# Kernel optimization log

Hardware: AMD Instinct MI355X
Metric: run time of the kernel (lower is better)

The kernel has to match this reference:

```python
import jax, jax.numpy as jnp
import numpy as np

D = 12  # grid size per axis (self.shape = [12,12,12])
BN_EPS = 1e-5


def _scatter(feats, idx, B):
    # feats: [N, C], idx: [N, 4] = (b, z, y, x). Coords are unique -> .set is exact.
    g = jnp.zeros((B, D, D, D, feats.shape[-1]), feats.dtype)
    return g.at[idx[:, 0], idx[:, 1], idx[:, 2], idx[:, 3]].set(feats)


def _subm_conv_bn_relu(feats, idx, B, W, b, gamma, beta):
    # Submanifold 3x3x3 conv == dense SAME conv on zero-filled grid, restricted
    # to the active sites (inactive neighbors contribute zero features).
    g = _scatter(feats, idx, B)  # [B, D, D, D, Cin]
    y = jax.lax.conv_general_dilated(
        g, W, window_strides=(1, 1, 1), padding='SAME',
        dimension_numbers=('NDHWC', 'DHWIO', 'NDHWC')) + b
    f = y[idx[:, 0], idx[:, 1], idx[:, 2], idx[:, 3]]  # gather active -> [N, Cout]
    # BatchNorm1d (training mode): biased batch stats over the N active points.
    mu = f.mean(axis=0)
    var = f.var(axis=0)
    f = (f - mu) * jax.lax.rsqrt(var + BN_EPS) * gamma + beta
    return jax.nn.relu(f)


def setup_inputs() -> dict:
    key = jax.random.key(0)
    B, per, Cin = 512, 864, 16
    N = B * per
    k_feat, k_coord, kp = jax.random.split(key, 3)
    # unique active voxels per batch element
    pkeys = jax.random.split(k_coord, B)
    lin = jax.vmap(lambda k: jax.random.permutation(k, D * D * D))(pkeys)[:, :per]  # [B, per]
    z, y, x = lin // (D * D), (lin // D) % D, lin % D
    bids = jnp.broadcast_to(jnp.arange(B)[:, None], (B, per))
    indices = jnp.stack([bids, z, y, x], axis=-1).reshape(N, 4).astype(jnp.int32)
    features = jax.random.normal(k_feat, (N, Cin), dtype=jnp.float32)
    ks = jax.random.split(kp, 6)
    inp = {
        'features': features, 'indices': indices, 'batch_size': B,
        'W0': jax.random.normal(ks[0], (3, 3, 3, Cin, 64), jnp.float32) * 0.05,
        'b0': jax.random.normal(ks[1], (64,), jnp.float32) * 0.05,
        'gamma0': jnp.ones((64,), jnp.float32), 'beta0': jnp.zeros((64,), jnp.float32),
        'W1': jax.random.normal(ks[2], (3, 3, 3, 64, 128), jnp.float32) * 0.05,
        'b1': jax.random.normal(ks[3], (128,), jnp.float32) * 0.05,
        'gamma1': jnp.ones((128,), jnp.float32), 'beta1': jnp.zeros((128,), jnp.float32),
        'W2': jax.random.normal(ks[4], (3, 3, 3, 128, 64), jnp.float32) * 0.05,
        'b2': jax.random.normal(ks[5], (64,), jnp.float32) * 0.05,
        'gamma2': jnp.ones((64,), jnp.float32), 'beta2': jnp.zeros((64,), jnp.float32),
    }
    return inp


def reference(features, indices, batch_size, W0, b0, gamma0, beta0,
              W1, b1, gamma1, beta1, W2, b2, gamma2, beta2):
    B = int(batch_size)
    f = _subm_conv_bn_relu(features, indices, B, W0, b0, gamma0, beta0)
    f = _subm_conv_bn_relu(f, indices, B, W1, b1, gamma1, beta1)
    f = _subm_conv_bn_relu(f, indices, B, W2, b2, gamma2, beta2)
    g = _scatter(f, indices, B)                 # [B, D, D, D, Cout]
    return jnp.transpose(g, (0, 4, 1, 2, 3))    # spconv .dense(): [B, C, D, H, W]
```

## Files before the change

kernel.cpp:

```cpp
#include <hip/hip_runtime.h>

#define DD 12
#define VOX 1728
#define BN_EPS 1e-5f
#define BATCH 512
#define PER 864
#define PERZ 865
#define NTOT (BATCH * PER)

typedef __attribute__((ext_vector_type(8))) short short8;
typedef __attribute__((ext_vector_type(4))) float f32x4;
typedef unsigned short u16;

__device__ inline u16 f2b(float f) {
    union { float f; unsigned u; } v; v.f = f;
    unsigned r = v.u + 0x7fffu + ((v.u >> 16) & 1u);
    return (u16)(r >> 16);
}
__device__ inline float b2f(u16 h) {
    union { unsigned u; float f; } v; v.u = ((unsigned)h) << 16;
    return v.f;
}
constexpr int ilog2(int v) { return v == 1 ? 0 : 1 + ilog2(v / 2); }

__device__ __forceinline__ void async_copy16(const void* g, void* l) {
    __builtin_amdgcn_global_load_lds(
        (const __attribute__((address_space(1))) void*)g,
        (__attribute__((address_space(3))) void*)l, 16, 0, 0);
}

template<int N> __device__ __forceinline__ void wait_vm() {
    if constexpr (N == 0)       asm volatile("s_waitcnt vmcnt(0)"  ::: "memory");
    else if constexpr (N == 8)  asm volatile("s_waitcnt vmcnt(8)"  ::: "memory");
    else if constexpr (N == 10) asm volatile("s_waitcnt vmcnt(10)" ::: "memory");
    else if constexpr (N == 12) asm volatile("s_waitcnt vmcnt(12)" ::: "memory");
    else if constexpr (N == 18) asm volatile("s_waitcnt vmcnt(18)" ::: "memory");
    else static_assert(N == 0, "unhandled vmcnt value");
}

__global__ void build_map_kernel(const int* __restrict__ idx, int* __restrict__ map, int N) {
    int p = blockIdx.x * blockDim.x + threadIdx.x;
    if (p >= N) return;
    const int4 v = ((const int4*)idx)[p];
    map[v.x * VOX + (v.y * DD + v.z) * DD + v.w] = p;
}

__global__ void build_nbr_kernel(const int* __restrict__ idx, const int* __restrict__ map,
                                 u16* __restrict__ nbr, int N) {
    int p = blockIdx.x * blockDim.x + threadIdx.x;
    if (p >= N) return;
    const int4 v = ((const int4*)idx)[p];
    const int base = v.x * VOX;
    const int lb = v.x * PER;
    #pragma unroll
    for (int nk = 0; nk < 27; nk++) {
        int dz = nk / 9 - 1, dy = (nk / 3) % 3 - 1, dx = nk % 3 - 1;
        int zz = v.y + dz, yy = v.z + dy, xx = v.w + dx;
        u16 out = PER;
        if (zz >= 0 && zz < DD && yy >= 0 && yy < DD && xx >= 0 && xx < DD) {
            int q = map[base + (zz * DD + yy) * DD + xx];
            if (q >= 0) out = (u16)(q - lb);
        }
        nbr[nk * N + p] = out;
    }
    #pragma unroll
    for (int nk = 27; nk < 32; nk++) nbr[nk * N + p] = PER;
}

__global__ void transpose_w_kernel(const float* __restrict__ W, u16* __restrict__ Wt,
                                   int K, int COUT, int Kpad) {
    int i = blockIdx.x * blockDim.x + threadIdx.x;
    if (i >= K * COUT) return;
    int n = i % COUT, k = i / COUT;
    Wt[(size_t)n * Kpad + k] = f2b(W[i]);
}

__global__ void cast_bf16_kernel(const float* __restrict__ in, u16* __restrict__ out, int total4) {
    int i = blockIdx.x * blockDim.x + threadIdx.x;
    if (i >= total4) return;
    int p = i >> 2, c4 = i & 3;
    int b = p / PERZ, r = p - b * PERZ;
    ushort4 o = make_ushort4(0, 0, 0, 0);
    if (r < PER) {
        float4 v = ((const float4*)in)[(size_t)(b * PER + r) * 4 + c4];
        o.x = f2b(v.x); o.y = f2b(v.y); o.z = f2b(v.z); o.w = f2b(v.w);
    }
    ((ushort4*)out)[i] = o;
}

template<int CIN, int COUT, int BM, int WM, int WN>
__global__ __launch_bounds__(256) void conv_mfma_kernel(
    const u16* __restrict__ fin,
    const u16* __restrict__ nbr,
    const u16* __restrict__ Wt,
    const float* __restrict__ bias,
    float* __restrict__ y,
    float* __restrict__ stats) {
    constexpr int Kpad   = (27 * CIN + 63) & ~63;
    constexpr int KSTEPS = Kpad / 64;
    constexpr int L2C    = ilog2(CIN);
    constexpr int BN     = WN * 64;
    constexpr int ASLOTS = BM / 32;
    constexpr int BSLOTS = BN / 32;
    constexpr int A_OFF  = BN * 128;
    constexpr int BUFB   = (BM + BN) * 128;
    static_assert(KSTEPS >= 3, "pipeline prologue needs >=3 K-steps");
    __shared__ char smem[2 * BUFB];

    const int perx = gridDim.x >> 3;
    const int bid = (blockIdx.x & 7) * perx + (blockIdx.x >> 3);
    const int p0 = bid * BM;

    const int tid = threadIdx.x;
    const int wave = tid >> 6, lane = tid & 63;
    const int wm = wave / WN, wn = wave % WN;
    const int lq = lane >> 4, lr = lane & 15;
    const int lrow = lane >> 3;
    const int kc_d = (lane & 7) ^ (lrow & 7);

    int qvoff[ASLOTS], gbase[ASLOTS];
    #pragma unroll
    for (int i = 0; i < ASLOTS; i++) {
        int m = (wave * ASLOTS + i) * 8 + lrow;
        int p = p0 + m;
        int b = p / PER;
        qvoff[i] = (((kc_d * 8) >> L2C) * NTOT + p) * 2;
        gbase[i] = b * PERZ * CIN + ((kc_d * 8) & (CIN - 1));
    }
    int bvoff[BSLOTS];
    #pragma unroll
    for (int j = 0; j < BSLOTS; j++)
        bvoff[j] = ((wave * BSLOTS + j) * 8 + lrow) * Kpad + kc_d * 8;

    int phs[2];
    phs[0] = ((0 + lq) ^ (lr & 7)) * 16;
    phs[1] = ((4 + lq) ^ (lr & 7)) * 16;
    const int aBase = A_OFF + (wm * 64 + lr) * 128;
    const int bBase = (wn * 64 + lr) * 128;

    const f32x4 fzero = {0.f, 0.f, 0.f, 0.f};
    f32x4 acc[4][4];
    #pragma unroll
    for (int i = 0; i < 4; i++)
        #pragma unroll
        for (int j = 0; j < 4; j++) acc[i][j] = fzero;

    u16 q[ASLOTS];
    auto loadQ = [&](int step) {
        int sQ = ((step * 64) >> L2C) * (NTOT * 2);
        #pragma unroll
        for (int i = 0; i < ASLOTS; i++)
            q[i] = *(const u16*)((const char*)nbr + qvoff[i] + sQ);
    };
    auto stage = [&](int step, int bo) {
        int sG = (step * 64) & (CIN - 1);
        const u16* fs = fin + sG;
        #pragma unroll
        for (int i = 0; i < ASLOTS; i++)
            async_copy16(fs + gbase[i] + ((int)q[i] << L2C),
                         smem + bo + A_OFF + (wave * ASLOTS + i) * 1024);
        const u16* wsrc = Wt + step * 64;
        #pragma unroll
        for (int j = 0; j < BSLOTS; j++)
            async_copy16(wsrc + bvoff[j], smem + bo + (wave * BSLOTS + j) * 1024);
    };

    loadQ(0);
    stage(0, 0);
    loadQ(1);

    #pragma unroll 1
    for (int kb = 0; kb < KSTEPS; kb++) {
        if (kb + 1 < KSTEPS) {
            stage(kb + 1, ((kb + 1) & 1) * BUFB);
            if (kb + 2 < KSTEPS) {
                loadQ(kb + 2);
                wait_vm<2 * ASLOTS + BSLOTS>();
            } else {
                wait_vm<ASLOTS + BSLOTS>();
            }
        } else {
            wait_vm<0>();
        }
        __builtin_amdgcn_s_barrier();

        const int so = (kb & 1) * BUFB;
        __builtin_amdgcn_s_setprio(1);
        #pragma unroll
        for (int s = 0; s < 2; s++) {
            short8 af[4], bfr[4];
            #pragma unroll
            for (int i = 0; i < 4; i++)
                af[i] = *(const short8*)(smem + so + aBase + i * 2048 + phs[s]);
            #pragma unroll
            for (int j = 0; j < 4; j++)
                bfr[j] = *(const short8*)(smem + so + bBase + j * 2048 + phs[s]);
            #pragma unroll
            for (int i = 0; i < 4; i++)
                #pragma unroll
                for (int j = 0; j < 4; j++)
                    acc[i][j] = __builtin_amdgcn_mfma_f32_16x16x32_bf16(af[i], bfr[j], acc[i][j], 0, 0, 0);
        }
        __builtin_amdgcn_s_setprio(0);
        asm volatile("s_waitcnt lgkmcnt(0)" ::: "memory");
        __builtin_amdgcn_s_barrier();
    }

    #pragma unroll
    for (int j = 0; j < 4; j++) {
        int col = wn * 64 + j * 16 + lr;
        float bv = bias[col];
        float s = 0.f, s2 = 0.f;
        #pragma unroll
        for (int i = 0; i < 4; i++) {
            int row0 = p0 + wm * 64 + i * 16 + lq * 4;
            #pragma unroll
            for (int r = 0; r < 4; r++) {
                float v = acc[i][j][r] + bv;
                y[(size_t)(row0 + r) * COUT + col] = v;
                s += v; s2 += v * v;
            }
        }
        s  += __shfl_down(s, 32);  s  += __shfl_down(s, 16);
        s2 += __shfl_down(s2, 32); s2 += __shfl_down(s2, 16);
        if (lane < 16) {
            atomicAdd(&stats[col], s);
            atomicAdd(&stats[COUT + col], s2);
        }
    }
}

template<int COUT>
__global__ void finalize_kernel(const float* __restrict__ stats, const float* __restrict__ gamma,
                                const float* __restrict__ beta, float* __restrict__ ss, int N) {
    int co = threadIdx.x;
    float inv_n = 1.f / (float)N;
    float mu  = stats[co] * inv_n;
    float var = stats[COUT + co] * inv_n - mu * mu;
    float sc  = gamma[co] * rsqrtf(var + BN_EPS);
    ss[co]        = sc;
    ss[COUT + co] = beta[co] - mu * sc;
}

template<int COUT>
__global__ void apply_kernel(const float* __restrict__ y, const float* __restrict__ ss,
                             u16* __restrict__ f, int total4) {
    int i = blockIdx.x * blockDim.x + threadIdx.x;
    if (i >= total4) return;
    constexpr int E4 = COUT / 4;
    int p = i / E4, k = i - p * E4;
    int b = p / PERZ, r = p - b * PERZ;
    ushort4 o = make_ushort4(0, 0, 0, 0);
    if (r < PER) {
        float4 v = ((const float4*)y)[(size_t)(b * PER + r) * E4 + k];
        int c0 = k * 4;
        float a;
        a = fmaf(v.x, ss[c0 + 0], ss[COUT + c0 + 0]); o.x = f2b(a > 0.f ? a : 0.f);
        a = fmaf(v.y, ss[c0 + 1], ss[COUT + c0 + 1]); o.y = f2b(a > 0.f ? a : 0.f);
        a = fmaf(v.z, ss[c0 + 2], ss[COUT + c0 + 2]); o.z = f2b(a > 0.f ? a : 0.f);
        a = fmaf(v.w, ss[c0 + 3], ss[COUT + c0 + 3]); o.w = f2b(a > 0.f ? a : 0.f);
    }
    ((ushort4*)f)[i] = o;
}

__global__ void output_kernel(const u16* __restrict__ f, const int* __restrict__ map,
                              float* __restrict__ out, int total) {
    int i = blockIdx.x * blockDim.x + threadIdx.x;
    if (i >= total) return;
    int voxel = i % VOX;
    int bc    = i / VOX;
    int c = bc & 63;
    int b = bc >> 6;
    int p = map[b * VOX + voxel];
    float v = 0.f;
    if (p >= 0) {
        int r = p - b * PER;
        v = b2f(f[(size_t)(b * PERZ + r) * 64 + c]);
    }
    out[i] = v;
}

__global__ void output_fused_kernel(const float* __restrict__ y, const float* __restrict__ ss,
                                    const int* __restrict__ map, float* __restrict__ out) {
    __shared__ float tile[64][65];
    __shared__ int   prow[64];
    const int chunk = blockIdx.x;
    const int b  = chunk / (VOX / 64);
    const int v0 = (chunk % (VOX / 64)) * 64;
    const int t = threadIdx.x;
    if (t < 64) prow[t] = map[b * VOX + v0 + t];
    __syncthreads();
    const int c = t & 63;
    const float sc = ss[c], sh = ss[64 + c];
    for (int v = t >> 6; v < 64; v += 4) {
        int p = prow[v];
        float val = 0.f;
        if (p >= 0) {
            float a = fmaf(y[(size_t)p * 64 + c], sc, sh);
            val = a > 0.f ? a : 0.f;
        }
        tile[v][c] = val;
    }
    __syncthreads();
    const int vv = t & 63;
    #pragma unroll
    for (int cc = t >> 6; cc < 64; cc += 4)
        out[(size_t)(b * 64 + cc) * VOX + v0 + vv] = tile[vv][cc];
}

extern "C" void kernel_launch(void* const* d_in, const int* in_sizes, int n_in,
                              void* d_out, int out_size, void* d_ws, size_t ws_size,
                              hipStream_t stream) {
    const float* feats = (const float*)d_in[0];
    const int*   idx   = (const int*)  d_in[1];
    const float* W0 = (const float*)d_in[3];
    const float* b0 = (const float*)d_in[4];
    const float* g0 = (const float*)d_in[5];
    const float* e0 = (const float*)d_in[6];
    const float* W1 = (const float*)d_in[7];
    const float* b1 = (const float*)d_in[8];
    const float* g1 = (const float*)d_in[9];
    const float* e1 = (const float*)d_in[10];
    const float* W2 = (const float*)d_in[11];
    const float* b2 = (const float*)d_in[12];
    const float* g2 = (const float*)d_in[13];
    const float* e2 = (const float*)d_in[14];

    const int N = in_sizes[0] / 16;

    char* ws = (char*)d_ws;
    size_t off = 0;
    auto alloc = [&](size_t bytes) { void* p = ws + off; off = (off + bytes + 255) & ~(size_t)255; return p; };
    int*   map   = (int*)  alloc((size_t)BATCH * VOX * 4);
    float* stats = (float*)alloc(3 * 256 * 4);
    float* ss    = (float*)alloc(3 * 256 * 4);
    u16*   nbr   = (u16*)  alloc((size_t)N * 32 * 2);
    u16*   wt0   = (u16*)  alloc((size_t)64  * 448  * 2);
    u16*   wt1   = (u16*)  alloc((size_t)128 * 1728 * 2);
    u16*   wt2   = (u16*)  alloc((size_t)64  * 3456 * 2);
    u16*   fbuf  = (u16*)  alloc((size_t)BATCH * PERZ * 128 * 2);
    float* y = (float*)d_out;

    const size_t y3_bytes = (size_t)N * 64 * 4;
    float* y3 = nullptr;
    if (off + y3_bytes <= ws_size) y3 = (float*)alloc(y3_bytes);

    hipMemsetAsync(map,   0xFF, (size_t)BATCH * VOX * 4, stream);
    hipMemsetAsync(stats, 0,    3 * 256 * 4, stream);
    hipMemsetAsync(wt0,   0,    (size_t)64 * 448 * 2, stream);
    build_map_kernel<<<(N + 255) / 256, 256, 0, stream>>>(idx, map, N);
    build_nbr_kernel<<<(N + 255) / 256, 256, 0, stream>>>(idx, map, nbr, N);
    transpose_w_kernel<<<(432  * 64  + 255) / 256, 256, 0, stream>>>(W0, wt0, 432,  64,  448);
    transpose_w_kernel<<<(1728 * 128 + 255) / 256, 256, 0, stream>>>(W1, wt1, 1728, 128, 1728);
    transpose_w_kernel<<<(3456 * 64  + 255) / 256, 256, 0, stream>>>(W2, wt2, 3456, 64,  3456);

    cast_bf16_kernel<<<(BATCH * PERZ * 4 + 255) / 256, 256, 0, stream>>>(feats, fbuf, BATCH * PERZ * 4);
    conv_mfma_kernel<16, 64, 256, 4, 1><<<N / 256, 256, 0, stream>>>(fbuf, nbr, wt0, b0, y, stats + 0);
    finalize_kernel<64><<<1, 64, 0, stream>>>(stats + 0, g0, e0, ss + 0, N);
    apply_kernel<64><<<(BATCH * PERZ * 16 + 255) / 256, 256, 0, stream>>>(y, ss + 0, fbuf, BATCH * PERZ * 16);

    conv_mfma_kernel<64, 128, 128, 2, 2><<<N / 128, 256, 0, stream>>>(fbuf, nbr, wt1, b1, y, stats + 256);
    finalize_kernel<128><<<1, 128, 0, stream>>>(stats + 256, g1, e1, ss + 256, N);
    apply_kernel<128><<<(BATCH * PERZ * 32 + 255) / 256, 256, 0, stream>>>(y, ss + 256, fbuf, BATCH * PERZ * 32);

    float* yL3 = y3 ? y3 : y;
    conv_mfma_kernel<128, 64, 256, 4, 1><<<N / 256, 256, 0, stream>>>(fbuf, nbr, wt2, b2, yL3, stats + 512);
    finalize_kernel<64><<<1, 64, 0, stream>>>(stats + 512, g2, e2, ss + 512, N);

    if (y3) {
        output_fused_kernel<<<BATCH * (VOX / 64), 256, 0, stream>>>(y3, ss + 512, map, (float*)d_out);
    } else {
        apply_kernel<64><<<(BATCH * PERZ * 16 + 255) / 256, 256, 0, stream>>>(y, ss + 512, fbuf, BATCH * PERZ * 16);
        output_kernel<<<(out_size + 255) / 256, 256, 0, stream>>>(fbuf, map, (float*)d_out, out_size);
    }
}
```

Before: 1.193 ms.

## Add 512-thread conv kernel with 128-wide K steps for layers 1 and 2

Adds a new implicit-GEMM conv kernel with 512-thread blocks, a 256x64 output tile and K steps of 128. It double-buffers the gathered A tile and single-buffers the weight B tile, and prefetches neighbour indices two steps ahead. Layers 1 and 2 switch to it; layer 1 splits its 128 output columns across two blocks, and its weight matrix is re-padded to a multiple of 128. The goal is fewer K iterations and barriers, plus higher occupancy and latency hiding for the gather. The cost is that the A gather is repeated for each column group in layer 1, and there is more pressure on LDS.

Measured after the change: 1.632 ms. 36.8% more time.

```diff
diff --git a/kernel.cpp b/kernel.cpp
--- a/kernel.cpp
+++ b/kernel.cpp
@@ -33,7 +33,7 @@
     if constexpr (N == 0)       asm volatile("s_waitcnt vmcnt(0)"  ::: "memory");
     else if constexpr (N == 8)  asm volatile("s_waitcnt vmcnt(8)"  ::: "memory");
     else if constexpr (N == 10) asm volatile("s_waitcnt vmcnt(10)" ::: "memory");
-    else if constexpr (N == 12) asm volatile("s_waitcnt vmcnt(12)" ::: "memory");
+    else if constexpr (N == 16) asm volatile("s_waitcnt vmcnt(16)" ::: "memory");
     else if constexpr (N == 18) asm volatile("s_waitcnt vmcnt(18)" ::: "memory");
     else static_assert(N == 0, "unhandled vmcnt value");
 }
@@ -90,12 +90,8 @@
 
 template<int CIN, int COUT, int BM, int WM, int WN>
 __global__ __launch_bounds__(256) void conv_mfma_kernel(
-    const u16* __restrict__ fin,
-    const u16* __restrict__ nbr,
-    const u16* __restrict__ Wt,
-    const float* __restrict__ bias,
-    float* __restrict__ y,
-    float* __restrict__ stats) {
+    const u16* __restrict__ fin, const u16* __restrict__ nbr, const u16* __restrict__ Wt,
+    const float* __restrict__ bias, float* __restrict__ y, float* __restrict__ stats) {
     constexpr int Kpad   = (27 * CIN + 63) & ~63;
     constexpr int KSTEPS = Kpad / 64;
     constexpr int L2C    = ilog2(CIN);
@@ -214,6 +210,153 @@
         #pragma unroll
         for (int i = 0; i < 4; i++) {
             int row0 = p0 + wm * 64 + i * 16 + lq * 4;
+            #pragma unroll
+            for (int r = 0; r < 4; r++) {
+                float v = acc[i][j][r] + bv;
+                y[(size_t)(row0 + r) * COUT + col] = v;
+                s += v; s2 += v * v;
+            }
+        }
+        s  += __shfl_down(s, 32);  s  += __shfl_down(s, 16);
+        s2 += __shfl_down(s2, 32); s2 += __shfl_down(s2, 16);
+        if (lane < 16) {
+            atomicAdd(&stats[col], s);
+            atomicAdd(&stats[COUT + col], s2);
+        }
+    }
+}
+
+template<int CIN, int COUT, int NG>
+__global__ __launch_bounds__(512) void conv512_kernel(
+    const u16* __restrict__ fin,
+    const u16* __restrict__ nbr,
+    const u16* __restrict__ Wt,
+    const float* __restrict__ bias,
+    float* __restrict__ y,
+    float* __restrict__ stats) {
+    constexpr int Kpad   = (27 * CIN + 127) & ~127;
+    constexpr int KSTEPS = Kpad / 128;
+    constexpr int TPT    = 128 / CIN;
+    constexpr int BM     = 256, BN = 64;
+    constexpr int ABUF   = BM * 256;
+    constexpr int BOFF   = 2 * ABUF;
+    static_assert(KSTEPS >= 3, "pipeline prologue needs >=3 K-steps");
+    __shared__ char smem[2 * ABUF + BN * 256];
+
+    const int perx = gridDim.x >> 3;
+    const int bid = (blockIdx.x & 7) * perx + (blockIdx.x >> 3);
+    const int colg = (NG > 1) ? (bid & (NG - 1)) : 0;
+    const int rowb = (NG > 1) ? (bid >> 1) : bid;
+    const int p0 = rowb * BM;
+
+    const int tid = threadIdx.x;
+    const int wave = tid >> 6, lane = tid & 63;
+    const int lq = lane >> 4, lr = lane & 15;
+    const int cph = lane & 15;
+
+    const char* nbrB = (const char*)nbr;
+    const char* finB = (const char*)fin;
+    const char* WtB  = (const char*)Wt;
+
+    int qvoff[8], gbase[8];
+    #pragma unroll
+    for (int i = 0; i < 8; i++) {
+        int rloc = i * 4 + lq;
+        int cl   = cph ^ (rloc & 15);
+        int p    = p0 + wave * 32 + rloc;
+        int b    = p / PER;
+        int tstep = (cl * 8) / CIN;
+        qvoff[i] = (tstep * NTOT + p) * 2;
+        gbase[i] = (b * PERZ * CIN + ((cl * 8) & (CIN - 1))) * 2;
+    }
+    int bvoff[2];
+    #pragma unroll
+    for (int j = 0; j < 2; j++) {
+        int rb = (wave * 2 + j) * 4 + lq;
+        int cl = cph ^ (rb & 15);
+        int n  = colg * 64 + rb;
+        bvoff[j] = (n * Kpad + cl * 8) * 2;
+    }
+
+    const f32x4 fzero = {0.f, 0.f, 0.f, 0.f};
+    f32x4 acc[2][4];
+    #pragma unroll
+    for (int i = 0; i < 2; i++)
+        #pragma unroll
+        for (int j = 0; j < 4; j++) acc[i][j] = fzero;
+
+    u16 q[8];
+    auto loadQ = [&](int step) {
+        int sQ = step * (TPT * NTOT * 2);
+        #pragma unroll
+        for (int i = 0; i < 8; i++)
+            q[i] = *(const u16*)(nbrB + qvoff[i] + sQ);
+    };
+    auto stageA = [&](int bo) {
+        #pragma unroll
+        for (int i = 0; i < 8; i++)
+            async_copy16(finB + gbase[i] + (int)q[i] * (CIN * 2),
+                         smem + bo + (wave * 8 + i) * 1024 + lane * 16);
+    };
+    auto stageB = [&](int step) {
+        const char* wsrc = WtB + step * 256;
+        #pragma unroll
+        for (int j = 0; j < 2; j++)
+            async_copy16(wsrc + bvoff[j], smem + BOFF + (wave * 2 + j) * 1024 + lane * 16);
+    };
+    const int aRow = wave * 32 + lr;
+    auto compute = [&](int bo) {
+        #pragma unroll
+        for (int s = 0; s < 4; s++) {
+            const int cx = ((s * 4 + lq) ^ lr) * 16;
+            short8 af[2], bfr[4];
+            #pragma unroll
+            for (int i = 0; i < 2; i++)
+                af[i] = *(const short8*)(smem + bo + (aRow + i * 16) * 256 + cx);
+            #pragma unroll
+            for (int j = 0; j < 4; j++)
+                bfr[j] = *(const short8*)(smem + BOFF + (j * 16 + lr) * 256 + cx);
+            #pragma unroll
+            for (int i = 0; i < 2; i++)
+                #pragma unroll
+                for (int j = 0; j < 4; j++)
+                    acc[i][j] = __builtin_amdgcn_mfma_f32_16x16x32_bf16(af[i], bfr[j], acc[i][j], 0, 0, 0);
+        }
+    };
+
+    loadQ(0);
+    stageA(0);
+    stageB(0);
+    loadQ(1);
+
+    #pragma unroll 1
+    for (int kb = 0; kb < KSTEPS; kb++) {
+        if (kb + 1 < KSTEPS) stageA(((kb + 1) & 1) * ABUF);
+        if (kb + 2 < KSTEPS) loadQ(kb + 2);
+        if (kb + 1 < KSTEPS) {
+            if (kb + 2 < KSTEPS) wait_vm<16>();
+            else                 wait_vm<8>();
+        } else {
+            wait_vm<0>();
+        }
+        __builtin_amdgcn_s_barrier();
+
+        __builtin_amdgcn_s_setprio(1);
+        compute((kb & 1) * ABUF);
+        __builtin_amdgcn_s_setprio(0);
+        asm volatile("s_waitcnt lgkmcnt(0)" ::: "memory");
+        __builtin_amdgcn_s_barrier();
+        if (kb + 1 < KSTEPS) stageB(kb + 1);
+    }
+
+    #pragma unroll
+    for (int j = 0; j < 4; j++) {
+        int col = colg * 64 + j * 16 + lr;
+        float bv = bias[col];
+        float s = 0.f, s2 = 0.f;
+        #pragma unroll
+        for (int i = 0; i < 2; i++) {
+            int row0 = p0 + wave * 32 + i * 16 + lq * 4;
             #pragma unroll
             for (int r = 0; r < 4; r++) {
                 float v = acc[i][j][r] + bv;
@@ -336,7 +479,7 @@
     float* ss    = (float*)alloc(3 * 256 * 4);
     u16*   nbr   = (u16*)  alloc((size_t)N * 32 * 2);
     u16*   wt0   = (u16*)  alloc((size_t)64  * 448  * 2);
-    u16*   wt1   = (u16*)  alloc((size_t)128 * 1728 * 2);
+    u16*   wt1   = (u16*)  alloc((size_t)128 * 1792 * 2);
     u16*   wt2   = (u16*)  alloc((size_t)64  * 3456 * 2);
     u16*   fbuf  = (u16*)  alloc((size_t)BATCH * PERZ * 128 * 2);
     float* y = (float*)d_out;
@@ -347,11 +490,12 @@
 
     hipMemsetAsync(map,   0xFF, (size_t)BATCH * VOX * 4, stream);
     hipMemsetAsync(stats, 0,    3 * 256 * 4, stream);
-    hipMemsetAsync(wt0,   0,    (size_t)64 * 448 * 2, stream);
+    hipMemsetAsync(wt0,   0,    (size_t)64  * 448  * 2, stream);
+    hipMemsetAsync(wt1,   0,    (size_t)128 * 1792 * 2, stream);
     build_map_kernel<<<(N + 255) / 256, 256, 0, stream>>>(idx, map, N);
     build_nbr_kernel<<<(N + 255) / 256, 256, 0, stream>>>(idx, map, nbr, N);
     transpose_w_kernel<<<(432  * 64  + 255) / 256, 256, 0, stream>>>(W0, wt0, 432,  64,  448);
-    transpose_w_kernel<<<(1728 * 128 + 255) / 256, 256, 0, stream>>>(W1, wt1, 1728, 128, 1728);
+    transpose_w_kernel<<<(1728 * 128 + 255) / 256, 256, 0, stream>>>(W1, wt1, 1728, 128, 1792);
     transpose_w_kernel<<<(3456 * 64  + 255) / 256, 256, 0, stream>>>(W2, wt2, 3456, 64,  3456);
 
     cast_bf16_kernel<<<(BATCH * PERZ * 4 + 255) / 256, 256, 0, stream>>>(feats, fbuf, BATCH * PERZ * 4);
@@ -359,12 +503,12 @@
     finalize_kernel<64><<<1, 64, 0, stream>>>(stats + 0, g0, e0, ss + 0, N);
     apply_kernel<64><<<(BATCH * PERZ * 16 + 255) / 256, 256, 0, stream>>>(y, ss + 0, fbuf, BATCH * PERZ * 16);
 
-    conv_mfma_kernel<64, 128, 128, 2, 2><<<N / 128, 256, 0, stream>>>(fbuf, nbr, wt1, b1, y, stats + 256);
+    conv512_kernel<64, 128, 2><<<(N / 256) * 2, 512, 0, stream>>>(fbuf, nbr, wt1, b1, y, stats + 256);
     finalize_kernel<128><<<1, 128, 0, stream>>>(stats + 256, g1, e1, ss + 256, N);
     apply_kernel<128><<<(BATCH * PERZ * 32 + 255) / 256, 256, 0, stream>>>(y, ss + 256, fbuf, BATCH * PERZ * 32);
 
     float* yL3 = y3 ? y3 : y;
-    conv_mfma_kernel<128, 64, 256, 4, 1><<<N / 256, 256, 0, stream>>>(fbuf, nbr, wt2, b2, yL3, stats + 512);
+    conv512_kernel<128, 64, 1><<<N / 256, 512, 0, stream>>>(fbuf, nbr, wt2, b2, yL3, stats + 512);
     finalize_kernel<64><<<1, 64, 0, stream>>>(stats + 512, g2, e2, ss + 512, N);
 
     if (y3) {
```
